# Kernel optimization log

Hardware: AMD Instinct MI355X
Metric: run time of the kernel (lower is better)

Reference implementation:

```python
import jax, jax.numpy as jnp
import numpy as np

LN_EPS = 1e-5

def _layernorm(x, g, b):
    mu = jnp.mean(x, axis=-1, keepdims=True)
    var = jnp.var(x, axis=-1, keepdims=True)
    return (x - mu) * jax.lax.rsqrt(var + LN_EPS) * g + b

def setup_inputs() -> dict:
    key = jax.random.key(0)
    ks = jax.random.split(key, 8)
    B, L, d_atom, d_hid = 8, 128, 256, 32
    return {
        "z":    jax.random.normal(ks[0], (B, L, d_atom), dtype=jnp.float32),
        "W_in": jax.random.normal(ks[1], (d_atom, 2 * d_hid), dtype=jnp.float32) * 0.02,
        "b_in": jnp.zeros((2 * d_hid,), dtype=jnp.float32),
        "ln_g": jnp.ones((2 * d_hid,), dtype=jnp.float32),
        "ln_b": jnp.zeros((2 * d_hid,), dtype=jnp.float32),
        "W1":   jax.random.normal(ks[2], (d_hid * d_hid, 21), dtype=jnp.float32) * 0.02,
        "b1":   jnp.zeros((21,), dtype=jnp.float32),
        "W2":   jax.random.normal(ks[3], (d_hid * d_hid, 30), dtype=jnp.float32) * 0.02,
        "b2":   jnp.zeros((30,), dtype=jnp.float32),
    }

def reference(z, W_in, b_in, ln_g, ln_b, W1, b1, W2, b2):
    # linear_in: Linear -> exact GELU -> LayerNorm
    ab = _layernorm(jax.nn.gelu(z @ W_in + b_in, approximate=False), ln_g, ln_b)
    h = ab.shape[-1] // 2
    a, b = ab[..., :h], ab[..., h:]              # (B, L, h) each
    # Fused bilinear form: outer(a_l, b_m) flattened to h*h, then Linear.
    # Equivalent to materializing (B, L, L, h*h) and matmul, reassociated.
    W1r = W1.reshape(h, h, -1)                   # (h, h, 21)
    W2r = W2.reshape(h, h, -1)                   # (h, h, 30)
    x1 = jnp.einsum('blc,bmd,cdk->blmk', a, b, W1r) + b1  # (B, L, L, 21)
    x2 = jnp.einsum('blc,bmd,cdk->blmk', a, b, W2r) + b2  # (B, L, L, 30)
    return (x1, x2)
```

## Files before the change

### kernel.cpp

```cpp
#include <hip/hip_runtime.h>
#include <hip/hip_bf16.h>
#include <math.h>

#define NB 8
#define NL 128
#define D_ATOM 256
#define DH 32
#define DAB 64
#define K1 21
#define K2 30
#define KT 51
#define ROWS (NB*NL)
#define LN_EPS 1e-5f

#define OUT1_ROW (NL*K1)
#define OUT2_ROW (NL*K2)
#define STAGE_N  (OUT1_ROW + OUT2_ROW)
#define TROW_HW 2048

typedef __attribute__((ext_vector_type(8))) short bf16x8;
typedef __attribute__((ext_vector_type(4))) float f32x4;

__device__ __forceinline__ unsigned short f2bf(float x) {
    __hip_bfloat16 h = __float2bfloat16(x);
    return *reinterpret_cast<unsigned short*>(&h);
}

__global__ __launch_bounds__(256) void ln_t_kernel(
    const float* __restrict__ z, const float* __restrict__ W_in,
    const float* __restrict__ b_in, const float* __restrict__ ln_g,
    const float* __restrict__ ln_b, const float* __restrict__ W1,
    const float* __restrict__ W2, unsigned short* __restrict__ bbf,
    unsigned short* __restrict__ T_ws)
{
    __shared__ float Wl[D_ATOM * DAB];
    __shared__ float zl[4][D_ATOM];
    __shared__ float al[4][DH];
    const int t = threadIdx.x;
    const int w = t >> 6, j = t & 63;
    const int row0 = blockIdx.x * 4;

    #pragma unroll
    for (int s = 0; s < 16; ++s) {
        int i4 = t + s * 256;
        ((float4*)Wl)[i4] = ((const float4*)W_in)[i4];
    }
    ((float4*)zl)[t] = ((const float4*)(z + (size_t)row0 * D_ATOM))[t];
    __syncthreads();

    float acc = b_in[j];
    #pragma unroll 8
    for (int i = 0; i < D_ATOM; ++i)
        acc = fmaf(zl[w][i], Wl[i * DAB + j], acc);

    float g = 0.5f * acc * (1.0f + erff(acc * 0.70710678118654752f));

    float s = g, sq = g * g;
    #pragma unroll
    for (int msk = 1; msk < 64; msk <<= 1) {
        s  += __shfl_xor(s,  msk, 64);
        sq += __shfl_xor(sq, msk, 64);
    }
    float mu  = s  * (1.0f / 64.0f);
    float var = sq * (1.0f / 64.0f) - mu * mu;
    float y = (g - mu) * rsqrtf(var + LN_EPS) * ln_g[j] + ln_b[j];

    const int row = row0 + w;
    if (j < DH) {
        al[w][j] = y;
    } else {
        const int d = j - DH, m = row & 127, batch = row >> 7;
        bbf[batch * 4096 + ((m >> 4) << 9) +
            ((((m & 15) | ((d >> 3) << 4)) << 3) | (d & 7))] = f2bf(y);
    }
    __syncthreads();

    float tacc[7][4];
    const float* wptr[7];
    int wstr[7], fidx[7];
    bool val[7];
    #pragma unroll
    for (int s2 = 0; s2 < 7; ++s2) {
        int o = t + s2 * 256;
        val[s2] = (o < 1632);
        int oo = val[s2] ? o : 0;
        int d, k;
        if (oo < 672) {
            wptr[s2] = W1 + oo; wstr[s2] = 672;
            d = oo / 21; k = oo % 21;
        } else {
            int o2 = oo - 672;
            wptr[s2] = W2 + o2; wstr[s2] = 960;
            d = o2 / 30; k = 21 + o2 % 30;
        }
        fidx[s2] = ((k >> 4) << 9) + ((((k & 15) | ((d >> 3) << 4)) << 3) | (d & 7));
        #pragma unroll
        for (int rr = 0; rr < 4; ++rr) tacc[s2][rr] = 0.f;
    }
    #pragma unroll 4
    for (int c = 0; c < DH; ++c) {
        float a0 = al[0][c], a1 = al[1][c], a2 = al[2][c], a3 = al[3][c];
        #pragma unroll
        for (int s2 = 0; s2 < 7; ++s2) {
            float wv = wptr[s2][c * wstr[s2]];
            tacc[s2][0] = fmaf(a0, wv, tacc[s2][0]);
            tacc[s2][1] = fmaf(a1, wv, tacc[s2][1]);
            tacc[s2][2] = fmaf(a2, wv, tacc[s2][2]);
            tacc[s2][3] = fmaf(a3, wv, tacc[s2][3]);
        }
    }
    #pragma unroll
    for (int s2 = 0; s2 < 7; ++s2) {
        if (val[s2]) {
            #pragma unroll
            for (int rr = 0; rr < 4; ++rr)
                T_ws[(size_t)(row0 + rr) * TROW_HW + fidx[s2]] = f2bf(tacc[s2][rr]);
        }
    }
}

__global__ __launch_bounds__(256) void pair_kernel(
    const unsigned short* __restrict__ bbf, const unsigned short* __restrict__ T_ws,
    const float* __restrict__ b1v, const float* __restrict__ b2v,
    float* __restrict__ out)
{
    const int row0  = blockIdx.x * 2;
    const int batch = row0 >> 7;
    const int t     = threadIdx.x;
    const int w = t >> 6, l = t & 63;
    const int lg = l >> 4, li = l & 15;
    const int r = w >> 1;
    const int mh = w & 1;

    __shared__ __align__(16) float stg[2][STAGE_N];

    bf16x8 afr[4], bfr[4];
    #pragma unroll
    for (int i = 0; i < 4; ++i)
        afr[i] = ((const bf16x8*)bbf)[batch * 512 + (mh * 4 + i) * 64 + l];
    #pragma unroll
    for (int kt = 0; kt < 4; ++kt)
        bfr[kt] = ((const bf16x8*)T_ws)[(size_t)(row0 + r) * 256 + kt * 64 + l];

    if (li >= 3) {
        bf16x8 zz = {0, 0, 0, 0, 0, 0, 0, 0};
        bfr[3] = zz;
    }

    float bias[4];
    #pragma unroll
    for (int kt = 0; kt < 4; ++kt) {
        int k = kt * 16 + li;
        bias[kt] = (k < K1) ? b1v[k] : (k < KT ? b2v[k - K1] : 0.f);
    }

    #pragma unroll
    for (int i = 0; i < 4; ++i) {
        const int mbase = (mh * 4 + i) * 16 + lg * 4;
        #pragma unroll
        for (int kt = 0; kt < 4; ++kt) {
            f32x4 acc = __builtin_amdgcn_mfma_f32_16x16x32_bf16(
                afr[i], bfr[kt], (f32x4){0.f, 0.f, 0.f, 0.f}, 0, 0, 0);
            const int k = kt * 16 + li;
            if (k < K1) {
                #pragma unroll
                for (int q = 0; q < 4; ++q)
                    stg[r][(mbase + q) * K1 + k] = acc[q] + bias[kt];
            } else if (k < KT) {
                #pragma unroll
                for (int q = 0; q < 4; ++q)
                    stg[r][OUT1_ROW + (mbase + q) * K2 + (k - K1)] = acc[q] + bias[kt];
            }
        }
    }
    __syncthreads();

    #pragma unroll
    for (int rr = 0; rr < 2; ++rr) {
        const int row = row0 + rr;
        float* o1 = out + (size_t)row * OUT1_ROW;
        float* o2 = out + (size_t)ROWS * OUT1_ROW + (size_t)row * OUT2_ROW;
        const float4* s1 = (const float4*)stg[rr];
        const float4* s2 = (const float4*)(stg[rr] + OUT1_ROW);
        for (int i4 = t; i4 < OUT1_ROW / 4; i4 += 256)
            ((float4*)o1)[i4] = s1[i4];
        for (int i4 = t; i4 < OUT2_ROW / 4; i4 += 256)
            ((float4*)o2)[i4] = s2[i4];
    }
}

extern "C" void kernel_launch(void* const* d_in, const int* in_sizes, int n_in,
                              void* d_out, int out_size, void* d_ws, size_t ws_size,
                              hipStream_t stream) {
    const float* z    = (const float*)d_in[0];
    const float* W_in = (const float*)d_in[1];
    const float* b_in = (const float*)d_in[2];
    const float* ln_g = (const float*)d_in[3];
    const float* ln_b = (const float*)d_in[4];
    const float* W1   = (const float*)d_in[5];
    const float* b1   = (const float*)d_in[6];
    const float* W2   = (const float*)d_in[7];
    const float* b2   = (const float*)d_in[8];
    float* out = (float*)d_out;

    unsigned short* bbf  = (unsigned short*)d_ws;
    unsigned short* T_ws = bbf + 32768;

    ln_t_kernel<<<256, 256, 0, stream>>>(z, W_in, b_in, ln_g, ln_b,
                                         W1, W2, bbf, T_ws);
    pair_kernel<<<ROWS / 2, 256, 0, stream>>>(bbf, T_ws, b1, b2, out);
}
```

Measured before the change: 26.65 us.

## Fuse both stages into one cooperative kernel with grid sync

Result: slower. 83.26 us (+212.4%).

```diff
diff --git a/kernel.cpp b/kernel.cpp
--- a/kernel.cpp
+++ b/kernel.cpp
@@ -1,6 +1,9 @@
 #include <hip/hip_runtime.h>
+#include <hip/hip_cooperative_groups.h>
 #include <hip/hip_bf16.h>
 #include <math.h>
+
+namespace cg = cooperative_groups;
 
 #define NB 8
 #define NL 128
@@ -16,7 +19,8 @@
 #define OUT1_ROW (NL*K1)
 #define OUT2_ROW (NL*K2)
 #define STAGE_N  (OUT1_ROW + OUT2_ROW)
-#define TROW_HW 2048
+#define WCAT 1632
+#define NWEL (DH*WCAT)
 
 typedef __attribute__((ext_vector_type(8))) short bf16x8;
 typedef __attribute__((ext_vector_type(4))) float f32x4;
@@ -26,113 +30,125 @@
     return *reinterpret_cast<unsigned short*>(&h);
 }
 
-__global__ __launch_bounds__(256) void ln_t_kernel(
+__global__ __launch_bounds__(256, 2) void fused_kernel(
     const float* __restrict__ z, const float* __restrict__ W_in,
     const float* __restrict__ b_in, const float* __restrict__ ln_g,
     const float* __restrict__ ln_b, const float* __restrict__ W1,
-    const float* __restrict__ W2, unsigned short* __restrict__ bbf,
-    unsigned short* __restrict__ T_ws)
-{
-    __shared__ float Wl[D_ATOM * DAB];
-    __shared__ float zl[4][D_ATOM];
-    __shared__ float al[4][DH];
-    const int t = threadIdx.x;
-    const int w = t >> 6, j = t & 63;
-    const int row0 = blockIdx.x * 4;
-
-    #pragma unroll
-    for (int s = 0; s < 16; ++s) {
-        int i4 = t + s * 256;
-        ((float4*)Wl)[i4] = ((const float4*)W_in)[i4];
-    }
-    ((float4*)zl)[t] = ((const float4*)(z + (size_t)row0 * D_ATOM))[t];
-    __syncthreads();
-
-    float acc = b_in[j];
-    #pragma unroll 8
-    for (int i = 0; i < D_ATOM; ++i)
-        acc = fmaf(zl[w][i], Wl[i * DAB + j], acc);
-
-    float g = 0.5f * acc * (1.0f + erff(acc * 0.70710678118654752f));
-
-    float s = g, sq = g * g;
-    #pragma unroll
-    for (int msk = 1; msk < 64; msk <<= 1) {
-        s  += __shfl_xor(s,  msk, 64);
-        sq += __shfl_xor(sq, msk, 64);
-    }
-    float mu  = s  * (1.0f / 64.0f);
-    float var = sq * (1.0f / 64.0f) - mu * mu;
-    float y = (g - mu) * rsqrtf(var + LN_EPS) * ln_g[j] + ln_b[j];
-
-    const int row = row0 + w;
-    if (j < DH) {
-        al[w][j] = y;
-    } else {
-        const int d = j - DH, m = row & 127, batch = row >> 7;
-        bbf[batch * 4096 + ((m >> 4) << 9) +
-            ((((m & 15) | ((d >> 3) << 4)) << 3) | (d & 7))] = f2bf(y);
-    }
-    __syncthreads();
-
-    float tacc[7][4];
-    const float* wptr[7];
-    int wstr[7], fidx[7];
-    bool val[7];
-    #pragma unroll
-    for (int s2 = 0; s2 < 7; ++s2) {
-        int o = t + s2 * 256;
-        val[s2] = (o < 1632);
-        int oo = val[s2] ? o : 0;
-        int d, k;
-        if (oo < 672) {
-            wptr[s2] = W1 + oo; wstr[s2] = 672;
-            d = oo / 21; k = oo % 21;
-        } else {
-            int o2 = oo - 672;
-            wptr[s2] = W2 + o2; wstr[s2] = 960;
-            d = o2 / 30; k = 21 + o2 % 30;
-        }
-        fidx[s2] = ((k >> 4) << 9) + ((((k & 15) | ((d >> 3) << 4)) << 3) | (d & 7));
-        #pragma unroll
-        for (int rr = 0; rr < 4; ++rr) tacc[s2][rr] = 0.f;
-    }
-    #pragma unroll 4
-    for (int c = 0; c < DH; ++c) {
-        float a0 = al[0][c], a1 = al[1][c], a2 = al[2][c], a3 = al[3][c];
-        #pragma unroll
-        for (int s2 = 0; s2 < 7; ++s2) {
-            float wv = wptr[s2][c * wstr[s2]];
-            tacc[s2][0] = fmaf(a0, wv, tacc[s2][0]);
-            tacc[s2][1] = fmaf(a1, wv, tacc[s2][1]);
-            tacc[s2][2] = fmaf(a2, wv, tacc[s2][2]);
-            tacc[s2][3] = fmaf(a3, wv, tacc[s2][3]);
-        }
-    }
-    #pragma unroll
-    for (int s2 = 0; s2 < 7; ++s2) {
-        if (val[s2]) {
-            #pragma unroll
-            for (int rr = 0; rr < 4; ++rr)
-                T_ws[(size_t)(row0 + rr) * TROW_HW + fidx[s2]] = f2bf(tacc[s2][rr]);
-        }
-    }
-}
-
-__global__ __launch_bounds__(256) void pair_kernel(
-    const unsigned short* __restrict__ bbf, const unsigned short* __restrict__ T_ws,
-    const float* __restrict__ b1v, const float* __restrict__ b2v,
+    const float* __restrict__ W2, const float* __restrict__ b1v,
+    const float* __restrict__ b2v, float* __restrict__ a_ws,
+    unsigned short* __restrict__ bbf, unsigned short* __restrict__ Wlin,
     float* __restrict__ out)
 {
-    const int row0  = blockIdx.x * 2;
+    __shared__ __align__(16) unsigned char smem[69632];
+    __shared__ float al[2][DH];
+
+    const int t   = threadIdx.x;
+    const int bid = blockIdx.x;
+
+    if (bid < 256) {
+        float* Wl  = (float*)smem;
+        float* zlf = (float*)(smem + 65536);
+        const int w = t >> 6, j = t & 63;
+        const int row0s = bid * 4;
+
+        #pragma unroll
+        for (int s = 0; s < 16; ++s) {
+            int i4 = t + s * 256;
+            ((float4*)Wl)[i4] = ((const float4*)W_in)[i4];
+        }
+        ((float4*)zlf)[t] = ((const float4*)(z + (size_t)row0s * D_ATOM))[t];
+        __syncthreads();
+
+        float acc = b_in[j];
+        #pragma unroll 8
+        for (int i = 0; i < D_ATOM; ++i)
+            acc = fmaf(zlf[w * D_ATOM + i], Wl[i * DAB + j], acc);
+
+        float g = 0.5f * acc * (1.0f + erff(acc * 0.70710678118654752f));
+
+        float s = g, sq = g * g;
+        #pragma unroll
+        for (int msk = 1; msk < 64; msk <<= 1) {
+            s  += __shfl_xor(s,  msk, 64);
+            sq += __shfl_xor(sq, msk, 64);
+        }
+        float mu  = s  * (1.0f / 64.0f);
+        float var = sq * (1.0f / 64.0f) - mu * mu;
+        float y = (g - mu) * rsqrtf(var + LN_EPS) * ln_g[j] + ln_b[j];
+
+        const int row = row0s + w;
+        if (j < DH) {
+            a_ws[row * DH + j] = y;
+        } else {
+            const int d = j - DH, m = row & 127, batch = row >> 7;
+            bbf[batch * 4096 + ((m >> 4) << 9) +
+                ((((m & 15) | ((d >> 3) << 4)) << 3) | (d & 7))] = f2bf(y);
+        }
+    } else if (bid < 307) {
+        const int base = (bid - 256) * 1024;
+        #pragma unroll
+        for (int e = 0; e < 4; ++e) {
+            int idx = base + e * 256 + t;
+            int c = idx / WCAT, o = idx - c * WCAT;
+            float v = (o < 672) ? W1[c * 672 + o] : W2[c * 960 + (o - 672)];
+            Wlin[idx] = f2bf(v);
+        }
+    }
+
+    cg::this_grid().sync();
+
+    unsigned short* Tf = (unsigned short*)smem;
+    float* stg = (float*)(smem + 8192);
+    const int row0  = bid * 2;
     const int batch = row0 >> 7;
-    const int t     = threadIdx.x;
-    const int w = t >> 6, l = t & 63;
+    const int w  = t >> 6, l = t & 63;
     const int lg = l >> 4, li = l & 15;
-    const int r = w >> 1;
+
+    #pragma unroll
+    for (int s = 0; s < 8; ++s)
+        ((unsigned int*)Tf)[t + s * 256] = 0u;
+    if (t < 2 * DH) al[t >> 5][t & 31] = a_ws[row0 * DH + t];
+    __syncthreads();
+
+    {
+        float tacc0[7], tacc1[7];
+        const unsigned short* wp[7];
+        int fidx[7];
+        bool val[7];
+        #pragma unroll
+        for (int s = 0; s < 7; ++s) {
+            int o = t + s * 256;
+            val[s] = (o < WCAT);
+            int oo = val[s] ? o : 0;
+            int d, k;
+            if (oo < 672) { d = oo / 21; k = oo % 21; }
+            else { int o2 = oo - 672; d = o2 / 30; k = 21 + o2 % 30; }
+            wp[s] = Wlin + oo;
+            fidx[s] = (((k >> 4) * 64 + ((k & 15) | ((d >> 3) << 4))) << 3) | (d & 7);
+            tacc0[s] = 0.f; tacc1[s] = 0.f;
+        }
+        #pragma unroll 4
+        for (int c = 0; c < DH; ++c) {
+            float ac0 = al[0][c], ac1 = al[1][c];
+            #pragma unroll
+            for (int s = 0; s < 7; ++s) {
+                float wv = __uint_as_float(((unsigned)wp[s][c * WCAT]) << 16);
+                tacc0[s] = fmaf(ac0, wv, tacc0[s]);
+                tacc1[s] = fmaf(ac1, wv, tacc1[s]);
+            }
+        }
+        #pragma unroll
+        for (int s = 0; s < 7; ++s) {
+            if (val[s]) {
+                Tf[fidx[s]]        = f2bf(tacc0[s]);
+                Tf[2048 + fidx[s]] = f2bf(tacc1[s]);
+            }
+        }
+    }
+    __syncthreads();
+
+    const int r  = w >> 1;
     const int mh = w & 1;
-
-    __shared__ __align__(16) float stg[2][STAGE_N];
 
     bf16x8 afr[4], bfr[4];
     #pragma unroll
@@ -140,12 +156,7 @@
         afr[i] = ((const bf16x8*)bbf)[batch * 512 + (mh * 4 + i) * 64 + l];
     #pragma unroll
     for (int kt = 0; kt < 4; ++kt)
-        bfr[kt] = ((const bf16x8*)T_ws)[(size_t)(row0 + r) * 256 + kt * 64 + l];
-
-    if (li >= 3) {
-        bf16x8 zz = {0, 0, 0, 0, 0, 0, 0, 0};
-        bfr[3] = zz;
-    }
+        bfr[kt] = ((const bf16x8*)Tf)[(r * 4 + kt) * 64 + l];
 
     float bias[4];
     #pragma unroll
@@ -154,6 +165,7 @@
         bias[kt] = (k < K1) ? b1v[k] : (k < KT ? b2v[k - K1] : 0.f);
     }
 
+    float* stg_r = stg + r * STAGE_N;
     #pragma unroll
     for (int i = 0; i < 4; ++i) {
         const int mbase = (mh * 4 + i) * 16 + lg * 4;
@@ -165,11 +177,11 @@
             if (k < K1) {
                 #pragma unroll
                 for (int q = 0; q < 4; ++q)
-                    stg[r][(mbase + q) * K1 + k] = acc[q] + bias[kt];
+                    stg_r[(mbase + q) * K1 + k] = acc[q] + bias[kt];
             } else if (k < KT) {
                 #pragma unroll
                 for (int q = 0; q < 4; ++q)
-                    stg[r][OUT1_ROW + (mbase + q) * K2 + (k - K1)] = acc[q] + bias[kt];
+                    stg_r[OUT1_ROW + (mbase + q) * K2 + (k - K1)] = acc[q] + bias[kt];
             }
         }
     }
@@ -180,8 +192,8 @@
         const int row = row0 + rr;
         float* o1 = out + (size_t)row * OUT1_ROW;
         float* o2 = out + (size_t)ROWS * OUT1_ROW + (size_t)row * OUT2_ROW;
-        const float4* s1 = (const float4*)stg[rr];
-        const float4* s2 = (const float4*)(stg[rr] + OUT1_ROW);
+        const float4* s1 = (const float4*)(stg + rr * STAGE_N);
+        const float4* s2 = (const float4*)(stg + rr * STAGE_N + OUT1_ROW);
         for (int i4 = t; i4 < OUT1_ROW / 4; i4 += 256)
             ((float4*)o1)[i4] = s1[i4];
         for (int i4 = t; i4 < OUT2_ROW / 4; i4 += 256)
@@ -203,10 +215,14 @@
     const float* b2   = (const float*)d_in[8];
     float* out = (float*)d_out;
 
-    unsigned short* bbf  = (unsigned short*)d_ws;
-    unsigned short* T_ws = bbf + 32768;
-
-    ln_t_kernel<<<256, 256, 0, stream>>>(z, W_in, b_in, ln_g, ln_b,
-                                         W1, W2, bbf, T_ws);
-    pair_kernel<<<ROWS / 2, 256, 0, stream>>>(bbf, T_ws, b1, b2, out);
+    float*          a_ws = (float*)d_ws;
+    unsigned short* bbf  = (unsigned short*)(a_ws + 32768);
+    unsigned short* Wlin = bbf + 32768;
+
+    void* args[] = { (void*)&z, (void*)&W_in, (void*)&b_in, (void*)&ln_g,
+                     (void*)&ln_b, (void*)&W1, (void*)&W2, (void*)&b1,
+                     (void*)&b2, (void*)&a_ws, (void*)&bbf, (void*)&Wlin,
+                     (void*)&out };
+    hipLaunchCooperativeKernel((const void*)fused_kernel, dim3(512), dim3(256),
+                               args, 0, stream);
 }
```
